# Kernel optimization log

Hardware: AMD Instinct MI355X
Metric: run time of the kernel (lower is better)

## Reference

```python
import jax, jax.numpy as jnp
import numpy as np

N = 50000
E = 500000
R = 8
IN_DIM = 128
HID = 128
OUT = 128
NUM_GRAPHS = 64
EPS_BN = 1e-5


def _glorot(key, shape):
    fan_in, fan_out = shape[-2], shape[-1]
    lim = np.sqrt(6.0 / (fan_in + fan_out))
    return jax.random.uniform(key, shape, jnp.float32, -lim, lim)


def setup_inputs() -> dict:
    key = jax.random.key(0)
    ks = jax.random.split(key, 24)
    x = jax.random.normal(ks[0], (N, IN_DIM), jnp.float32)
    edge_index = jax.random.randint(ks[1], (2, E), 0, N, jnp.int64)
    edge_type = jax.random.randint(ks[2], (E,), 0, R, jnp.int64)
    batch = jnp.sort(jax.random.randint(ks[3], (N,), 0, NUM_GRAPHS, jnp.int64))
    d = {
        "x": x, "edge_index": edge_index, "edge_type": edge_type, "batch": batch,
        # RGCN layer 1 (in->hid): per-relation weights, root weight, bias
        "W1": _glorot(ks[4], (R, IN_DIM, HID)), "root1": _glorot(ks[5], (IN_DIM, HID)), "b1": jnp.zeros((HID,), jnp.float32),
        "W2": _glorot(ks[6], (R, HID, HID)), "root2": _glorot(ks[7], (HID, HID)), "b2": jnp.zeros((HID,), jnp.float32),
        "W3": _glorot(ks[8], (R, HID, HID)), "root3": _glorot(ks[9], (HID, HID)), "b3": jnp.zeros((HID,), jnp.float32),
        # BatchNorm affine params
        "g1": jnp.ones((HID,), jnp.float32), "beta1": jnp.zeros((HID,), jnp.float32),
        "g2": jnp.ones((HID,), jnp.float32), "beta2": jnp.zeros((HID,), jnp.float32),
        # attention MLP: hid -> hid//2 -> 1
        "A1": _glorot(ks[10], (HID, HID // 2)), "a1": jnp.zeros((HID // 2,), jnp.float32),
        "A2": _glorot(ks[11], (HID // 2, 1)), "a2": jnp.zeros((1,), jnp.float32),
        # combiner MLP: 2*hid -> hid -> out
        "C1": _glorot(ks[12], (2 * HID, HID)), "c1": jnp.zeros((HID,), jnp.float32),
        "C2": _glorot(ks[13], (HID, OUT)), "c2": jnp.zeros((OUT,), jnp.float32),
    }
    return d


def rgcn_conv(h, src, dst, etype, W, root, bias):
    # relation-wise gather -> mean-aggregate per (dst, relation) -> transform
    seg = dst * R + etype                                   # [E]
    msg = h[src]                                            # [E, d_in] gather
    agg = jax.ops.segment_sum(msg, seg, num_segments=N * R) # [N*R, d_in]
    cnt = jax.ops.segment_sum(jnp.ones((seg.shape[0],), h.dtype), seg, num_segments=N * R)
    agg = agg / jnp.maximum(cnt, 1.0)[:, None]              # mean aggregation (PyG default)
    agg = agg.reshape(N, R, -1)
    out = jnp.einsum('nri,rio->no', agg, W) + h @ root + bias
    return out


def batch_norm(h, gamma, beta):
    mu = jnp.mean(h, axis=0, keepdims=True)
    var = jnp.mean((h - mu) ** 2, axis=0, keepdims=True)
    return (h - mu) * jax.lax.rsqrt(var + EPS_BN) * gamma + beta


def lrelu(h):
    return jax.nn.leaky_relu(h, 0.1)


def reference(x, edge_index, edge_type, batch, W1, root1, b1, W2, root2, b2,
              W3, root3, b3, g1, beta1, g2, beta2, A1, a1, A2, a2, C1, c1, C2, c2):
    src, dst = edge_index[0], edge_index[1]
    h = rgcn_conv(x, src, dst, edge_type, W1, root1, b1)
    h = lrelu(batch_norm(h, g1, beta1))
    h = rgcn_conv(h, src, dst, edge_type, W2, root2, b2)
    h = lrelu(batch_norm(h, g2, beta2))
    node_emb = rgcn_conv(h, src, dst, edge_type, W3, root3, b3)  # [N, HID]

    # attention pooling: scores softmax-ed over ALL nodes (dim=0, as in source)
    scores = lrelu(node_emb @ A1 + a1) @ A2 + a2                 # [N, 1]
    attn = jax.nn.softmax(scores, axis=0)                        # [N, 1]
    global_emb = jax.ops.segment_sum(node_emb * attn, batch, num_segments=NUM_GRAPHS)

    combined = jnp.concatenate([node_emb, global_emb[batch]], axis=1)  # [N, 2*HID]
    final = lrelu(combined @ C1 + c1) @ C2 + c2                  # [N, OUT]
    norm = jnp.linalg.norm(final, axis=1, keepdims=True)
    return final / jnp.maximum(norm, 1e-12)
```

## Files before the change

kernel.cpp:

```cpp
#include <hip/hip_runtime.h>
#include <hip/hip_bf16.h>

typedef unsigned int u32;
typedef unsigned short u16;
typedef __bf16 bf16_t;
typedef bf16_t bf16x8 __attribute__((ext_vector_type(8)));
typedef float f32x4 __attribute__((ext_vector_type(4)));

constexpr int NN = 50000;
constexpr int EE = 500000;
constexpr int RR = 8;
constexpr int NKEY = RR * NN;
constexpr int PAIR_B = (NKEY + 511) / 512;

constexpr int WX_A1T = 0;
constexpr int WX_C1T = 8192;
constexpr int WX_C2T = 40960;
constexpr int WX_A2  = 57344;
constexpr int WX_a1  = 57408;
constexpr int WX_c1  = 57472;
constexpr int WX_c2  = 57600;
constexpr int WX_a2s = 57728;
constexpr int WX_TOT = 57729;

__device__ __forceinline__ float bf2f(u32 v){
  union { u32 u; float f; } x; x.u = (v & 0xFFFFu) << 16; return x.f;
}
__device__ __forceinline__ u16 f2bf(float f){
  union { u32 u; float f; } x; x.f = f;
  u32 r = x.u + 0x7FFFu + ((x.u >> 16) & 1u);
  return (u16)(r >> 16);
}
__device__ __forceinline__ float lrelu(float x){ return x > 0.f ? x : 0.1f * x; }
__device__ __forceinline__ float ldf(const void* p, int i, u32 fm){
  return fm ? ((const float*)p)[i] : bf2f(((const u16*)p)[i]);
}
__device__ __forceinline__ void gl_lds16(const u16* g, u16* l){
  __builtin_amdgcn_global_load_lds((const __attribute__((address_space(1))) u32*)g,
                                   (__attribute__((address_space(3))) u32*)l, 16, 0, 0);
}
__device__ __forceinline__ bf16x8 cvt8(float4 a, float4 b){
  union { bf16x8 v; u16 s[8]; } r;
  r.s[0]=f2bf(a.x); r.s[1]=f2bf(a.y); r.s[2]=f2bf(a.z); r.s[3]=f2bf(a.w);
  r.s[4]=f2bf(b.x); r.s[5]=f2bf(b.y); r.s[6]=f2bf(b.z); r.s[7]=f2bf(b.w);
  return r.v;
}

__global__ void k_fdetect(const void* x, u32* md){
  __shared__ u32 c;
  if (threadIdx.x == 0) c = 0;
  __syncthreads();
  const u16* p = (const u16*)x;
  u32 loc = 0;
  for (int j = 0; j < 16; j++){
    u16 v = p[threadIdx.x * 16 + j];
    u32 e = (v >> 7) & 0xFF;
    if (e >= 0xFD) loc++;
  }
  atomicAdd(&c, loc);
  __syncthreads();
  if (threadIdx.x == 0) md[0] = (c >= 4) ? 1u : 0u;
}
__global__ void k_idetect(const void* et, u32* md){
  __shared__ u32 c;
  if (threadIdx.x == 0) c = 0;
  __syncthreads();
  const int* p = (const int*)et;
  u32 loc = 0;
  for (int j = 0; j < 8; j++){
    int idx = 2 * (threadIdx.x * 8 + j) + 1;
    if (p[idx] != 0) loc++;
  }
  atomicAdd(&c, loc);
  __syncthreads();
  if (threadIdx.x == 0) md[1] = (c == 0) ? 1u : 0u;
}

__global__ void k_icvt(const void* ei, const void* et, const void* bat,
                       int* ei_c, int* et_c, int* bat_c, u32* __restrict__ cnt,
                       const u32* md){
  u32 im = md[1];
  int i = blockIdx.x * 256 + threadIdx.x;
  if (i < EE){
    const int* p = (const int*)ei;
    ei_c[i] = im ? p[2 * i] : p[i];
  } else if (i < 2 * EE){
    int j = i - EE;
    const int* p = (const int*)ei;
    const int* pt = (const int*)et;
    int d = im ? p[2 * i] : p[i];
    int r = im ? pt[2 * j] : pt[j];
    ei_c[i] = d;
    atomicAdd(&cnt[d * RR + r], 1u);
  } else if (i < 3 * EE){
    int j = i - 2 * EE;
    const int* p = (const int*)et;
    et_c[j] = im ? p[2 * j] : p[j];
  } else if (i < 3 * EE + NN){
    int j = i - 3 * EE;
    const int* p = (const int*)bat;
    bat_c[j] = im ? p[2 * j] : p[j];
  }
}

__global__ void k_xcvt(const void* x, u16* xb, const u32* md, u32* flags){
  u32 fm = md[0];
  int i4 = (blockIdx.x * 256 + threadIdx.x) * 4;
  if (i4 >= NN * 128) return;
  float v[4];
  if (fm){
    float4 f = *(const float4*)((const float*)x + i4);
    v[0]=f.x; v[1]=f.y; v[2]=f.z; v[3]=f.w;
  } else {
    uint2 u = *(const uint2*)((const u16*)x + i4);
    v[0]=bf2f(u.x); v[1]=bf2f(u.x>>16); v[2]=bf2f(u.y); v[3]=bf2f(u.y>>16);
  }
  bool bad = false;
  u16 o[4];
  for (int j = 0; j < 4; j++){
    if (v[j] != v[j]){ bad = true; v[j] = 0.f; }
    o[j] = f2bf(v[j]);
  }
  unsigned long long bal = __ballot(bad);
  if (bal && (threadIdx.x & 63) == 0) atomicOr(flags, 2u);
  uint2 st;
  st.x = (u32)o[0] | ((u32)o[1] << 16);
  st.y = (u32)o[2] | ((u32)o[3] << 16);
  *(uint2*)(xb + i4) = st;
}

__global__ void k_wcat(const void* W1, const void* r1, const void* W2, const void* r2,
                       const void* W3, const void* r3, u16* wcatT, const u32* md, u32* flags){
  u32 fm = md[0];
  int idx = blockIdx.x * 256 + threadIdx.x;
  if (idx >= 3 * 128 * 1152) return;
  int L = idx / (128 * 1152);
  int rem = idx % (128 * 1152);
  int n = rem / 1152, k = rem % 1152;
  const void* W  = (L == 0) ? W1 : ((L == 1) ? W2 : W3);
  const void* rt = (L == 0) ? r1 : ((L == 1) ? r2 : r3);
  float v;
  if (k < 1024){
    int r = k & 7, c = k >> 3;
    v = ldf(W, (r * 128 + c) * 128 + n, fm);
  } else {
    v = ldf(rt, (k - 1024) * 128 + n, fm);
  }
  if (v != v){ v = 0.f; atomicOr(flags, 2u); }
  wcatT[idx] = f2bf(v);
}

__global__ void k_wext(const void* A1, const void* a1, const void* A2, const void* a2,
                       const void* C1, const void* c1, const void* C2, const void* c2,
                       u16* wext, const u32* md){
  u32 fm = md[0];
  int idx = blockIdx.x * 256 + threadIdx.x;
  if (idx >= WX_TOT) return;
  float v;
  if (idx < WX_C1T){
    int n = idx >> 7, k = idx & 127;
    v = ldf(A1, k * 64 + n, fm);
  } else if (idx < WX_C2T){
    int j = idx - WX_C1T; int n = j >> 8, k = j & 255;
    v = ldf(C1, k * 128 + n, fm);
  } else if (idx < WX_A2){
    int j = idx - WX_C2T; int n = j >> 7, k = j & 127;
    v = ldf(C2, k * 128 + n, fm);
  } else if (idx < WX_a1){ v = ldf(A2, idx - WX_A2, fm); }
  else if (idx < WX_c1){ v = ldf(a1, idx - WX_a1, fm); }
  else if (idx < WX_c2){ v = ldf(c1, idx - WX_c1, fm); }
  else if (idx < WX_a2s){ v = ldf(c2, idx - WX_c2, fm); }
  else { v = ldf(a2, 0, fm); }
  wext[idx] = f2bf(v);
}

__global__ void k_pairA(const u32* __restrict__ cnt, u32* __restrict__ blockSum){
  __shared__ u32 sd[256];
  int b = blockIdx.x, t = threadIdx.x;
  u32 s = 0;
  for (int j = 0; j < 2; j++){
    int key = b * 512 + t * 2 + j;
    if (key < NKEY) s += cnt[key];
  }
  sd[t] = s; __syncthreads();
  for (int off = 128; off; off >>= 1){ if (t < off) sd[t] += sd[t + off]; __syncthreads(); }
  if (t == 0) blockSum[b] = sd[0];
}
__global__ void k_pairB(const u32* __restrict__ blockSum, u32* __restrict__ blockBase){
  int lane = threadIdx.x;
  u32 loc[13]; u32 s = 0;
  for (int j = 0; j < 13; j++){
    int b = lane * 13 + j;
    u32 v = (b < PAIR_B) ? blockSum[b] : 0u;
    loc[j] = s; s += v;
  }
  u32 tot = s;
  for (int off = 1; off < 64; off <<= 1){
    u32 x = __shfl_up(tot, off);
    if (lane >= off) tot += x;
  }
  u32 excl = tot - s;
  for (int j = 0; j < 13; j++){
    int b = lane * 13 + j;
    if (b < PAIR_B) blockBase[b] = excl + loc[j];
  }
}
__global__ void k_pairC(const u32* __restrict__ cnt, const u32* __restrict__ blockBase,
                        u32* __restrict__ pairStart, u32* __restrict__ cursor){
  __shared__ u32 sd[256];
  int b = blockIdx.x, t = threadIdx.x;
  int k0 = b * 512 + t * 2;
  u32 v0 = 0, v1 = 0;
  if (k0 < NKEY) v0 = cnt[k0];
  if (k0 + 1 < NKEY) v1 = cnt[k0 + 1];
  sd[t] = v0 + v1; __syncthreads();
  for (int off = 1; off < 256; off <<= 1){
    u32 x = (t >= off) ? sd[t - off] : 0u;
    __syncthreads();
    sd[t] += x;
    __syncthreads();
  }
  u32 excl = sd[t] - (v0 + v1);
  u32 base = blockBase[b] + excl;
  if (k0 < NKEY){ pairStart[k0] = base; cursor[k0] = 0u; }
  if (k0 + 1 < NKEY){ pairStart[k0 + 1] = base + v0; cursor[k0 + 1] = 0u; }
  if (k0 + 1 == NKEY - 1) pairStart[NKEY] = base + v0 + v1;
}
__global__ void k_sort3(const int* __restrict__ ei, const int* __restrict__ et,
                        const u32* __restrict__ pairStart, u32* __restrict__ cursor,
                        u32* __restrict__ src_s){
  int e = blockIdx.x * 256 + threadIdx.x;
  if (e >= EE) return;
  int r = et[e], d = ei[EE + e];
  u32 key = (u32)d * RR + (u32)r;
  u32 p = pairStart[key] + atomicAdd(&cursor[key], 1u);
  src_s[p] = (u32)ei[e];
}

__global__ __launch_bounds__(256) void k_agg(const u16* __restrict__ h,
                                             const u32* __restrict__ pairStart,
                                             const u32* __restrict__ src_s,
                                             u16* __restrict__ agg){
  int d = blockIdx.x * 4 + (threadIdx.x >> 6);
  if (d >= NN) return;
  int lane = threadIdx.x & 63;
  const uint4* p4 = (const uint4*)(pairStart + d * 8);
  uint4 q0 = p4[0], q1 = p4[1];
  u32 ps[9];
  ps[0]=q0.x; ps[1]=q0.y; ps[2]=q0.z; ps[3]=q0.w;
  ps[4]=q1.x; ps[5]=q1.y; ps[6]=q1.z; ps[7]=q1.w;
  ps[8]=pairStart[d * 8 + 8];
  u32 jb = ps[0], je = ps[8];
  u32 pre = 0;
  if (jb + lane < je) pre = src_s[jb + lane];
  const u16* hb = h + lane * 2;
  u32 ou[8] = {0,0,0,0,0,0,0,0};
  #pragma unroll
  for (int r = 0; r < 8; r++){
    u32 s = ps[r], e = ps[r + 1];
    float a0 = 0.f, a1 = 0.f, b0 = 0.f, b1 = 0.f;
    u32 j = s;
    for (; j + 1 < e; j += 2){
      u32 i0 = j - jb;
      u32 s0 = (i0 < 64) ? __shfl(pre, (int)i0) : src_s[j];
      u32 s1 = (i0 + 1 < 64) ? __shfl(pre, (int)(i0 + 1)) : src_s[j + 1];
      u32 v0 = *(const u32*)(hb + (size_t)s0 * 128);
      u32 v1 = *(const u32*)(hb + (size_t)s1 * 128);
      a0 += bf2f(v0); a1 += bf2f(v0 >> 16);
      b0 += bf2f(v1); b1 += bf2f(v1 >> 16);
    }
    if (j < e){
      u32 i0 = j - jb;
      u32 s0 = (i0 < 64) ? __shfl(pre, (int)i0) : src_s[j];
      u32 v0 = *(const u32*)(hb + (size_t)s0 * 128);
      a0 += bf2f(v0); a1 += bf2f(v0 >> 16);
    }
    a0 += b0; a1 += b1;
    int c = (int)(e - s);
    float sc = 1.0f / (float)max(c, 1);
    u32 m0 = (u32)f2bf(a0 * sc), m1 = (u32)f2bf(a1 * sc);
    ou[r >> 1]       |= m0 << ((r & 1) * 16);
    ou[4 + (r >> 1)] |= m1 << ((r & 1) * 16);
  }
  uint4* dst = (uint4*)(agg + (size_t)d * 1024 + lane * 16);
  dst[0] = make_uint4(ou[0], ou[1], ou[2], ou[3]);
  dst[1] = make_uint4(ou[4], ou[5], ou[6], ou[7]);
}

__global__ __launch_bounds__(256) void k_gemm_big(const u16* __restrict__ h,
                                                  const u16* __restrict__ agg,
                                                  const u16* __restrict__ wT,
                                                  const void* __restrict__ bias,
                                                  float* __restrict__ out, const u32* md,
                                                  float* __restrict__ stats, int do_stats){
  __shared__ u16 As[2][64][64];
  __shared__ u16 Bs[2][128][64];
  u32 fm = md[0];
  int m0 = blockIdx.x * 64;
  int tid = threadIdx.x;
  int w = tid >> 6, lane = tid & 63, qd = lane >> 4, l16 = lane & 15;

  int rin = lane >> 3;
  int sc8 = (lane & 7) ^ rin;

  const u16* agA[2]; const u16* hA[2];
  #pragma unroll
  for (int i = 0; i < 2; i++){
    int row = (w * 2 + i) * 8 + rin;
    int node = m0 + row; if (node > NN - 1) node = NN - 1;
    agA[i] = agg + (size_t)node * 1024 + sc8 * 8;
    hA[i]  = h + (size_t)node * 128 + sc8 * 8;
  }
  const u16* wB[4];
  #pragma unroll
  for (int i = 0; i < 4; i++){
    int row = (w * 4 + i) * 8 + rin;
    wB[i] = wT + (size_t)row * 1152 + sc8 * 8;
  }

  auto stage = [&](int k0, int b){
    if (k0 < 1024){
      gl_lds16(agA[0] + k0, &As[b][(w * 2 + 0) * 8][0]);
      gl_lds16(agA[1] + k0, &As[b][(w * 2 + 1) * 8][0]);
    } else {
      gl_lds16(hA[0] + (k0 - 1024), &As[b][(w * 2 + 0) * 8][0]);
      gl_lds16(hA[1] + (k0 - 1024), &As[b][(w * 2 + 1) * 8][0]);
    }
    #pragma unroll
    for (int i = 0; i < 4; i++) gl_lds16(wB[i] + k0, &Bs[b][(w * 4 + i) * 8][0]);
  };

  f32x4 acc[8];
  #pragma unroll
  for (int j = 0; j < 8; j++) acc[j] = (f32x4){0.f,0.f,0.f,0.f};

  int sw = (l16 & 7) << 3;
  stage(0, 0);
  __syncthreads();
  for (int t = 0; t < 18; t++){
    int b = t & 1;
    if (t + 1 < 18) stage((t + 1) * 64, b ^ 1);
    #pragma unroll
    for (int kk = 0; kk < 64; kk += 32){
      bf16x8 a = *(const bf16x8*)(&As[b][w * 16 + l16][(kk + qd * 8) ^ sw]);
      #pragma unroll
      for (int ct = 0; ct < 8; ct++){
        bf16x8 bb = *(const bf16x8*)(&Bs[b][ct * 16 + l16][(kk + qd * 8) ^ sw]);
        acc[ct] = __builtin_amdgcn_mfma_f32_16x16x32_bf16(a, bb, acc[ct], 0, 0, 0);
      }
    }
    __syncthreads();
  }

  float sarr[8], s2arr[8];
  #pragma unroll
  for (int ct = 0; ct < 8; ct++){
    int col = ct * 16 + l16;
    float bv = ldf(bias, col, fm);
    float s = 0.f, s2 = 0.f;
    int rbase = m0 + w * 16 + qd * 4;
    #pragma unroll
    for (int rg = 0; rg < 4; rg++){
      int node = rbase + rg;
      if (node < NN){
        float v = acc[ct][rg] + bv;
        out[(size_t)node * 128 + col] = v;
        s += v; s2 += v * v;
      }
    }
    s  += __shfl_xor(s, 16);  s  += __shfl_xor(s, 32);
    s2 += __shfl_xor(s2, 16); s2 += __shfl_xor(s2, 32);
    sarr[ct] = s; s2arr[ct] = s2;
  }
  if (do_stats){
    float* red = (float*)&As[0][0][0];
    __syncthreads();
    if (qd == 0){
      #pragma unroll
      for (int ct = 0; ct < 8; ct++){
        red[w * 256 + ct * 16 + l16] = sarr[ct];
        red[w * 256 + 128 + ct * 16 + l16] = s2arr[ct];
      }
    }
    __syncthreads();
    if (tid < 256){
      float v = red[tid] + red[256 + tid] + red[512 + tid] + red[768 + tid];
      unsafeAtomicAdd(&stats[tid], v);
    }
  }
}

__global__ void k_bnapply(const float* __restrict__ out, const float* __restrict__ stats,
                          const void* __restrict__ g, const void* __restrict__ beta,
                          u16* __restrict__ hout, const u32* md, u32* flags, u32 layerbit){
  u32 fm = md[0];
  int idx = (blockIdx.x * 256 + threadIdx.x) * 4;
  if (idx >= NN * 128) return;
  int col = idx & 127;
  float4 v = *(const float4*)(out + idx);
  float vv[4] = {v.x, v.y, v.z, v.w};
  bool bad = false;
  u16 o[4];
  for (int j = 0; j < 4; j++){
    int c = col + j;
    float mu = stats[c] * (1.0f / NN);
    float var = fmaxf(stats[128 + c] * (1.0f / NN) - mu * mu, 0.f);
    float sc = ldf(g, c, fm) * rsqrtf(var + 1e-5f);
    float sh = ldf(beta, c, fm) - mu * sc;
    float r = vv[j] * sc + sh;
    if (r != r || sc != sc){ bad = true; r = 0.f; }
    o[j] = f2bf(lrelu(r));
  }
  unsigned long long bal = __ballot(bad);
  if (bal && (threadIdx.x & 63) == 0) atomicOr(flags, layerbit);
  uint2 st;
  st.x = (u32)o[0] | ((u32)o[1] << 16);
  st.y = (u32)o[2] | ((u32)o[3] << 16);
  *(uint2*)(hout + idx) = st;
}

__global__ __launch_bounds__(256) void k_scores_mfma(const float* __restrict__ emb,
                                                     const u16* __restrict__ wext,
                                                     float* __restrict__ scores, u32* smax){
  int m0 = blockIdx.x * 64;
  int tid = threadIdx.x;
  int w = tid >> 6, lane = tid & 63, qd = lane >> 4, l16 = lane & 15;
  int na = m0 + w * 16 + l16; if (na > NN - 1) na = NN - 1;
  const float* arow = emb + (size_t)na * 128;
  f32x4 acc[4];
  #pragma unroll
  for (int j = 0; j < 4; j++) acc[j] = (f32x4){0.f,0.f,0.f,0.f};
  #pragma unroll
  for (int k0 = 0; k0 < 4; k0++){
    float4 f0 = *(const float4*)(arow + k0 * 32 + qd * 8);
    float4 f1 = *(const float4*)(arow + k0 * 32 + qd * 8 + 4);
    bf16x8 a = cvt8(f0, f1);
    #pragma unroll
    for (int ct = 0; ct < 4; ct++){
      bf16x8 b = *(const bf16x8*)(wext + WX_A1T + (size_t)(ct * 16 + l16) * 128 + k0 * 32 + qd * 8);
      acc[ct] = __builtin_amdgcn_mfma_f32_16x16x32_bf16(a, b, acc[ct], 0, 0, 0);
    }
  }
  float a1v[4], a2v[4];
  #pragma unroll
  for (int ct = 0; ct < 4; ct++){
    a1v[ct] = bf2f(wext[WX_a1 + ct * 16 + l16]);
    a2v[ct] = bf2f(wext[WX_A2 + ct * 16 + l16]);
  }
  float a2s = bf2f(wext[WX_a2s]);
  float bm = -1e30f;
  #pragma unroll
  for (int rg = 0; rg < 4; rg++){
    float s = 0.f;
    #pragma unroll
    for (int ct = 0; ct < 4; ct++)
      s += lrelu(acc[ct][rg] + a1v[ct]) * a2v[ct];
    s += __shfl_xor(s, 1); s += __shfl_xor(s, 2);
    s += __shfl_xor(s, 4); s += __shfl_xor(s, 8);
    int row = m0 + w * 16 + qd * 4 + rg;
    float sf = s + a2s;
    if (row < NN){
      bm = fmaxf(bm, sf);
      if (l16 == 0) scores[row] = sf;
    }
  }
  bm = fmaxf(bm, __shfl_xor(bm, 16));
  bm = fmaxf(bm, __shfl_xor(bm, 32));
  if (lane == 0) atomicMax(smax, (bm >= -1e29f) ?
      ((__float_as_uint(bm) & 0x80000000u) ? ~__float_as_uint(bm) : (__float_as_uint(bm) | 0x80000000u)) : 0u);
}

__device__ __forceinline__ float funmap(u32 m){
  union{u32 u; float f;} x;
  x.u = (m & 0x80000000u) ? (m ^ 0x80000000u) : ~m;
  return x.f;
}

__global__ void k_expsum(const float* __restrict__ scores, const u32* smax,
                         float* __restrict__ attnw, float* ssum, u32* flags){
  float mx = funmap(*smax);
  int gid = blockIdx.x * 256 + threadIdx.x;
  if (mx != mx){ if (gid == 0) atomicOr(flags, 32u); mx = 0.f; }
  float s = 0.f;
  bool bad = false;
  for (int i = gid; i < NN; i += 256 * 128){
    float e = __expf(scores[i] - mx);
    if (e != e){ bad = true; e = 0.f; }
    attnw[i] = e; s += e;
  }
  unsigned long long bal = __ballot(bad);
  if (bal && (threadIdx.x & 63) == 0) atomicOr(flags, 32u);
  for (int off = 32; off; off >>= 1) s += __shfl_down(s, off);
  if ((threadIdx.x & 63) == 0) unsafeAtomicAdd(ssum, s);
}

constexpr int POOL_CHUNK = 32;
__global__ __launch_bounds__(128) void k_pool(const float* __restrict__ emb,
                                              const float* __restrict__ attnw,
                                              const float* __restrict__ ssum,
                                              const int* __restrict__ batch,
                                              float* __restrict__ gemb, u32* flags){
  int t = threadIdx.x;
  int n0 = blockIdx.x * POOL_CHUNK;
  if (n0 >= NN) return;
  int n1 = min(n0 + POOL_CHUNK, NN);
  float sv = *ssum;
  bool bad = !(sv > 0.f) || (sv != sv);
  if (bad && t == 0 && blockIdx.x == 0) atomicOr(flags, 64u);
  float rs = bad ? 0.f : 1.0f / sv;
  int cur = batch[n0];
  float acc = 0.f;
  for (int n = n0; n < n1; n++){
    int b = batch[n];
    if (b != cur){ unsafeAtomicAdd(&gemb[cur * 128 + t], acc * rs); acc = 0.f; cur = b; }
    acc += emb[(size_t)n * 128 + t] * attnw[n];
  }
  unsafeAtomicAdd(&gemb[cur * 128 + t], acc * rs);
}

__global__ void k_gembC(const float* __restrict__ gemb, const u16* __restrict__ wext,
                        float* __restrict__ gembC){
  int idx = blockIdx.x * 256 + threadIdx.x;
  if (idx >= 64 * 128) return;
  int g = idx >> 7, n = idx & 127;
  const float* gr = gemb + g * 128;
  const u16* wr = wext + WX_C1T + (size_t)n * 256 + 128;
  float s = 0.f;
  #pragma unroll 8
  for (int k = 0; k < 128; k++) s += gr[k] * bf2f(wr[k]);
  gembC[idx] = s + bf2f(wext[WX_c1 + n]);
}

__global__ __launch_bounds__(256) void k_final_mfma(const float* __restrict__ emb,
                                                    const float* __restrict__ gembC,
                                                    const int* __restrict__ batch,
                                                    const u16* __restrict__ wext,
                                                    void* __restrict__ outp,
                                                    const u32* md){
  __shared__ u16 Hs[64][136];
  u32 fm = md[0];
  int m0 = blockIdx.x * 64;
  int tid = threadIdx.x;
  int w = tid >> 6, lane = tid & 63, qd = lane >> 4, l16 = lane & 15;
  int na = m0 + w * 16 + l16; if (na > NN - 1) na = NN - 1;
  const float* arow = emb + (size_t)na * 128;

  f32x4 acc[8];
  #pragma unroll
  for (int j = 0; j < 8; j++) acc[j] = (f32x4){0.f,0.f,0.f,0.f};
  #pragma unroll
  for (int k0 = 0; k0 < 4; k0++){
    float4 f0 = *(const float4*)(arow + k0 * 32 + qd * 8);
    float4 f1 = *(const float4*)(arow + k0 * 32 + qd * 8 + 4);
    bf16x8 a = cvt8(f0, f1);
    #pragma unroll
    for (int ct = 0; ct < 8; ct++){
      bf16x8 b = *(const bf16x8*)(wext + WX_C1T + (size_t)(ct * 16 + l16) * 256 + k0 * 32 + qd * 8);
      acc[ct] = __builtin_amdgcn_mfma_f32_16x16x32_bf16(a, b, acc[ct], 0, 0, 0);
    }
  }
  int rbase = w * 16 + qd * 4;
  int gg[4];
  #pragma unroll
  for (int rg = 0; rg < 4; rg++){
    int node = m0 + rbase + rg; if (node > NN - 1) node = NN - 1;
    gg[rg] = batch[node];
  }
  #pragma unroll
  for (int ct = 0; ct < 8; ct++){
    int col = ct * 16 + l16;
    #pragma unroll
    for (int rg = 0; rg < 4; rg++){
      float h = acc[ct][rg] + gembC[gg[rg] * 128 + col];
      Hs[rbase + rg][col] = f2bf(lrelu(h));
    }
  }
  __syncthreads();
  f32x4 acc2[8];
  #pragma unroll
  for (int j = 0; j < 8; j++) acc2[j] = (f32x4){0.f,0.f,0.f,0.f};
  #pragma unroll
  for (int k0 = 0; k0 < 4; k0++){
    bf16x8 a = *(const bf16x8*)(&Hs[w * 16 + l16][k0 * 32 + qd * 8]);
    #pragma unroll
    for (int ct = 0; ct < 8; ct++){
      bf16x8 b = *(const bf16x8*)(wext + WX_C2T + (size_t)(ct * 16 + l16) * 128 + k0 * 32 + qd * 8);
      acc2[ct] = __builtin_amdgcn_mfma_f32_16x16x32_bf16(a, b, acc2[ct], 0, 0, 0);
    }
  }
  float c2v[8];
  #pragma unroll
  for (int ct = 0; ct < 8; ct++) c2v[ct] = bf2f(wext[WX_c2 + ct * 16 + l16]);
  #pragma unroll
  for (int rg = 0; rg < 4; rg++){
    float ss = 0.f;
    #pragma unroll
    for (int ct = 0; ct < 8; ct++){
      float o = acc2[ct][rg] + c2v[ct];
      ss += o * o;
    }
    ss += __shfl_xor(ss, 1); ss += __shfl_xor(ss, 2);
    ss += __shfl_xor(ss, 4); ss += __shfl_xor(ss, 8);
    float sc = 1.0f / fmaxf(sqrtf(ss), 1e-12f);
    int row = m0 + rbase + rg;
    if (row < NN){
      if (fm){
        float* op = (float*)outp;
        #pragma unroll
        for (int ct = 0; ct < 8; ct++)
          op[(size_t)row * 128 + ct * 16 + l16] = (acc2[ct][rg] + c2v[ct]) * sc;
      } else {
        u16* op = (u16*)outp;
        #pragma unroll
        for (int ct = 0; ct < 8; ct++)
          op[(size_t)row * 128 + ct * 16 + l16] = f2bf((acc2[ct][rg] + c2v[ct]) * sc);
      }
    }
  }
}

__global__ void k_diag(const u32* pairStart, const u32* flags, const u32* md, void* outp){
  if (threadIdx.x != 0 || blockIdx.x != 0) return;
  u32 fm = md[0];
  u32 f = flags[0];
  if (pairStart[NKEY] != (u32)EE) f |= 1u;
  for (int b = 0; b < 9; b++){
    if (f & (1u << b)){
      float s = (float)(131072 >> b);
      if (fm) ((float*)outp)[b] = s;
      else ((u16*)outp)[b] = f2bf(s);
    }
  }
}
__global__ void k_wsfail(u32* outp){ outp[0] = 0x43000000u; }

constexpr size_t O_OUT   = 0;
constexpr size_t O_H     = 25600000;
constexpr size_t O_XBF   = 38400000;
constexpr size_t O_WCAT  = 51200000;
constexpr size_t O_WEXT  = 52084736;
constexpr size_t O_EI    = 52200448;
constexpr size_t O_ET    = 56200448;
constexpr size_t O_BAT   = 58200448;
constexpr size_t O_SRC   = 58400448;
constexpr size_t O_PST   = 60400448;
constexpr size_t O_GEMBC = 62100448;
constexpr size_t O_CNT   = 62400448;
constexpr size_t O_SCO   = 65600448;
constexpr size_t O_AW    = 65800448;
constexpr size_t O_GEMB  = 66000448;
constexpr size_t O_STATS = 66033216;
constexpr size_t O_MISC  = 66035264;
constexpr size_t O_AGG   = 66035520;
constexpr size_t WS_NEED = 168435520;

extern "C" void kernel_launch(void* const* d_in, const int* in_sizes, int n_in,
                              void* d_out, int out_size, void* d_ws, size_t ws_size,
                              hipStream_t stream) {
  const void* x     = d_in[0];
  const void* ei    = d_in[1];
  const void* et    = d_in[2];
  const void* batch = d_in[3];
  const void* W1 = d_in[4],  *r1 = d_in[5],  *b1 = d_in[6];
  const void* W2 = d_in[7],  *r2 = d_in[8],  *b2 = d_in[9];
  const void* W3 = d_in[10], *r3 = d_in[11], *b3 = d_in[12];
  const void* g1 = d_in[13], *be1 = d_in[14];
  const void* g2 = d_in[15], *be2 = d_in[16];
  const void* A1 = d_in[17], *a1 = d_in[18];
  const void* A2 = d_in[19], *a2 = d_in[20];
  const void* C1 = d_in[21], *c1 = d_in[22];
  const void* C2 = d_in[23], *c2 = d_in[24];

  if (ws_size < WS_NEED){ k_wsfail<<<1, 1, 0, stream>>>((u32*)d_out); return; }
  char* ws = (char*)d_ws;
  float* out   = (float*)(ws + O_OUT);
  u16*   hbuf  = (u16*)(ws + O_H);
  u16*   xbf   = (u16*)(ws + O_XBF);
  u16*   wcat  = (u16*)(ws + O_WCAT);
  u16*   wext  = (u16*)(ws + O_WEXT);
  int*   ei_c  = (int*)(ws + O_EI);
  int*   et_c  = (int*)(ws + O_ET);
  int*   bat_c = (int*)(ws + O_BAT);
  u32*   src_s = (u32*)(ws + O_SRC);
  u32*   pairStart = (u32*)(ws + O_PST);
  float* gembC = (float*)(ws + O_GEMBC);
  u32*   cnt   = (u32*)(ws + O_CNT);
  float* sco   = (float*)(ws + O_SCO);
  float* aw    = (float*)(ws + O_AW);
  float* gemb  = (float*)(ws + O_GEMB);
  float* stats = (float*)(ws + O_STATS);
  u32*   misc  = (u32*)(ws + O_MISC);
  u16*   aggb  = (u16*)(ws + O_AGG);
  u32* cursor    = (u32*)(ws + O_OUT);
  u32* blockSum  = (u32*)(ws + O_OUT + 1600000);
  u32* blockBase = (u32*)(ws + O_OUT + 1604096);
  u32* smax = misc + 25;
  float* ssum = (float*)(misc + 26);
  u32* flags = misc + 27;
  u32* md = misc + 28;

  hipMemsetAsync(ws + O_CNT, 0, 1600000, stream);
  hipMemsetAsync(ws + O_GEMB, 0, 32768 + 2048 + 256, stream);

  k_fdetect<<<1, 256, 0, stream>>>(x, md);
  k_idetect<<<1, 256, 0, stream>>>(et, md);
  k_icvt<<<6055, 256, 0, stream>>>(ei, et, batch, ei_c, et_c, bat_c, cnt, md);
  k_xcvt<<<6250, 256, 0, stream>>>(x, xbf, md, flags);
  k_wcat<<<1728, 256, 0, stream>>>(W1, r1, W2, r2, W3, r3, wcat, md, flags);
  k_wext<<<227, 256, 0, stream>>>(A1, a1, A2, a2, C1, c1, C2, c2, wext, md);

  k_pairA<<<PAIR_B, 256, 0, stream>>>(cnt, blockSum);
  k_pairB<<<1, 64, 0, stream>>>(blockSum, blockBase);
  k_pairC<<<PAIR_B, 256, 0, stream>>>(cnt, blockBase, pairStart, cursor);
  k_sort3<<<(EE + 255) / 256, 256, 0, stream>>>(ei_c, et_c, pairStart, cursor, src_s);

  const void* bias[3] = {b1, b2, b3};
  const void* gam[2] = {g1, g2};
  const void* bet[2] = {be1, be2};
  const u16* hin = xbf;
  for (int L = 0; L < 3; L++){
    const u16* wT = wcat + (size_t)L * 128 * 1152;
    k_agg<<<(NN + 3) / 4, 256, 0, stream>>>(hin, pairStart, src_s, aggb);
    k_gemm_big<<<(NN + 63) / 64, 256, 0, stream>>>(hin, aggb, wT, bias[L], out, md,
                                                   stats + (L < 2 ? L * 256 : 0), (L < 2) ? 1 : 0);
    if (L < 2){
      k_bnapply<<<6250, 256, 0, stream>>>(out, stats + L * 256, gam[L], bet[L], hbuf, md, flags, 4u << L);
      hin = hbuf;
    }
  }
  k_scores_mfma<<<(NN + 63) / 64, 256, 0, stream>>>(out, wext, sco, smax);
  k_expsum<<<128, 256, 0, stream>>>(sco, smax, aw, ssum, flags);
  k_pool<<<(NN + POOL_CHUNK - 1) / POOL_CHUNK, 128, 0, stream>>>(out, aw, ssum, bat_c, gemb, flags);
  k_gembC<<<32, 256, 0, stream>>>(gemb, wext, gembC);
  k_final_mfma<<<(NN + 63) / 64, 256, 0, stream>>>(out, gembC, bat_c, wext, d_out, md);
  k_diag<<<1, 64, 0, stream>>>(pairStart, flags, md, d_out);
}
```

Baseline: 697.7 us.

## Use single-buffered K=128 tiles in big RGCN GEMM instead of double-buffered K=64

The big GEMM kernel now loads K-tiles of 128 into a single LDS buffer and syncs before and after each load, replacing the double-buffered K=64 pipeline. The loop trip count drops from 18 to 9, which halves the barriers and gives more MFMA work per tile, but global-to-LDS loads no longer overlap with compute. LDS use per block stays the same, and the swizzle pattern is adjusted for 128-wide rows.

```diff
diff --git a/kernel.cpp b/kernel.cpp
--- a/kernel.cpp
+++ b/kernel.cpp
@@ -293,63 +293,63 @@
                                                   const void* __restrict__ bias,
                                                   float* __restrict__ out, const u32* md,
                                                   float* __restrict__ stats, int do_stats){
-  __shared__ u16 As[2][64][64];
-  __shared__ u16 Bs[2][128][64];
+  __shared__ u16 As[64][128];
+  __shared__ u16 Bs[128][128];
   u32 fm = md[0];
   int m0 = blockIdx.x * 64;
   int tid = threadIdx.x;
   int w = tid >> 6, lane = tid & 63, qd = lane >> 4, l16 = lane & 15;
 
-  int rin = lane >> 3;
-  int sc8 = (lane & 7) ^ rin;
-
-  const u16* agA[2]; const u16* hA[2];
-  #pragma unroll
-  for (int i = 0; i < 2; i++){
-    int row = (w * 2 + i) * 8 + rin;
+  int rin4 = lane >> 4;
+  int c16 = lane & 15;
+
+  const u16* agA[4];
+  #pragma unroll
+  for (int i = 0; i < 4; i++){
+    int row = (w * 4 + i) * 4 + rin4;
     int node = m0 + row; if (node > NN - 1) node = NN - 1;
+    int sc8 = c16 ^ (4 * (i & 1) + rin4);
     agA[i] = agg + (size_t)node * 1024 + sc8 * 8;
-    hA[i]  = h + (size_t)node * 128 + sc8 * 8;
-  }
-  const u16* wB[4];
-  #pragma unroll
-  for (int i = 0; i < 4; i++){
-    int row = (w * 4 + i) * 8 + rin;
+  }
+  const u16* wB[8];
+  #pragma unroll
+  for (int i = 0; i < 8; i++){
+    int row = (w * 8 + i) * 4 + rin4;
+    int sc8 = c16 ^ (4 * (i & 1) + rin4);
     wB[i] = wT + (size_t)row * 1152 + sc8 * 8;
   }
 
-  auto stage = [&](int k0, int b){
+  f32x4 acc[8];
+  #pragma unroll
+  for (int j = 0; j < 8; j++) acc[j] = (f32x4){0.f,0.f,0.f,0.f};
+
+  int sw = (l16 & 7) << 3;
+  for (int k0 = 0; k0 < 1152; k0 += 128){
+    __syncthreads();
     if (k0 < 1024){
-      gl_lds16(agA[0] + k0, &As[b][(w * 2 + 0) * 8][0]);
-      gl_lds16(agA[1] + k0, &As[b][(w * 2 + 1) * 8][0]);
+      #pragma unroll
+      for (int i = 0; i < 4; i++) gl_lds16(agA[i] + k0, &As[(w * 4 + i) * 4][0]);
     } else {
-      gl_lds16(hA[0] + (k0 - 1024), &As[b][(w * 2 + 0) * 8][0]);
-      gl_lds16(hA[1] + (k0 - 1024), &As[b][(w * 2 + 1) * 8][0]);
-    }
-    #pragma unroll
-    for (int i = 0; i < 4; i++) gl_lds16(wB[i] + k0, &Bs[b][(w * 4 + i) * 8][0]);
-  };
-
-  f32x4 acc[8];
-  #pragma unroll
-  for (int j = 0; j < 8; j++) acc[j] = (f32x4){0.f,0.f,0.f,0.f};
-
-  int sw = (l16 & 7) << 3;
-  stage(0, 0);
-  __syncthreads();
-  for (int t = 0; t < 18; t++){
-    int b = t & 1;
-    if (t + 1 < 18) stage((t + 1) * 64, b ^ 1);
-    #pragma unroll
-    for (int kk = 0; kk < 64; kk += 32){
-      bf16x8 a = *(const bf16x8*)(&As[b][w * 16 + l16][(kk + qd * 8) ^ sw]);
+      #pragma unroll
+      for (int i = 0; i < 4; i++){
+        int row = (w * 4 + i) * 4 + rin4;
+        int node = m0 + row; if (node > NN - 1) node = NN - 1;
+        int sc8 = c16 ^ (4 * (i & 1) + rin4);
+        gl_lds16(h + (size_t)node * 128 + sc8 * 8, &As[(w * 4 + i) * 4][0]);
+      }
+    }
+    #pragma unroll
+    for (int i = 0; i < 8; i++) gl_lds16(wB[i] + k0, &Bs[(w * 8 + i) * 4][0]);
+    __syncthreads();
+    #pragma unroll
+    for (int kk = 0; kk < 128; kk += 32){
+      bf16x8 a = *(const bf16x8*)(&As[w * 16 + l16][(kk + qd * 8) ^ sw]);
       #pragma unroll
       for (int ct = 0; ct < 8; ct++){
-        bf16x8 bb = *(const bf16x8*)(&Bs[b][ct * 16 + l16][(kk + qd * 8) ^ sw]);
+        bf16x8 bb = *(const bf16x8*)(&Bs[ct * 16 + l16][(kk + qd * 8) ^ sw]);
         acc[ct] = __builtin_amdgcn_mfma_f32_16x16x32_bf16(a, bb, acc[ct], 0, 0, 0);
       }
     }
-    __syncthreads();
   }
 
   float sarr[8], s2arr[8];
@@ -373,7 +373,7 @@
     sarr[ct] = s; s2arr[ct] = s2;
   }
   if (do_stats){
-    float* red = (float*)&As[0][0][0];
+    float* red = (float*)&As[0][0];
     __syncthreads();
     if (qd == 0){
       #pragma unroll
```

Result: faster. 651.4 us (-6.6%).
